# Kernel tuning notes

Hardware: AMD Instinct MI355X
Metric: run time of the kernel (lower is better)

The kernel has to match this reference:

```python
import jax, jax.numpy as jnp
import numpy as np

HEADS = 4
HEAD_DIM = 32
NEG_SLOPE = 0.2  # PyG GATConv default

N_NODES = 100000
N_EDGES = 1600000
IN_CH = 128
N_GRAPHS = 64


def setup_inputs() -> dict:
    key = jax.random.key(0)
    ks = jax.random.split(key, 6)
    x = jax.random.normal(ks[0], (N_NODES, IN_CH), dtype=jnp.float32)
    edge_index = jax.random.randint(ks[1], (2, N_EDGES), 0, N_NODES, dtype=jnp.int32)
    batch = jnp.sort(jax.random.randint(ks[2], (N_NODES,), 0, N_GRAPHS, dtype=jnp.int32))
    # glorot-style scaling
    W = jax.random.normal(ks[3], (IN_CH, HEADS * HEAD_DIM), dtype=jnp.float32) * (1.0 / np.sqrt(IN_CH))
    att_src = jax.random.normal(ks[4], (HEADS, HEAD_DIM), dtype=jnp.float32) * (1.0 / np.sqrt(HEAD_DIM))
    att_dst = jax.random.normal(ks[5], (HEADS, HEAD_DIM), dtype=jnp.float32) * (1.0 / np.sqrt(HEAD_DIM))
    bias = jnp.zeros((HEADS * HEAD_DIM,), dtype=jnp.float32)
    return {"x": x, "edge_index": edge_index, "batch": batch,
            "W": W, "att_src": att_src, "att_dst": att_dst, "bias": bias}


def reference(x, edge_index, batch, W, att_src, att_dst, bias):
    # batch is unused (collect_embeddings=False path); kept for signature fidelity
    N = x.shape[0]
    # add self-loops (PyG GATConv default add_self_loops=True)
    loop = jnp.arange(N, dtype=edge_index.dtype)
    src = jnp.concatenate([edge_index[0], loop])  # [E+N]
    dst = jnp.concatenate([edge_index[1], loop])  # [E+N]

    # linear transform, split heads: [N, H, C]
    xt = (x @ W).reshape(N, HEADS, HEAD_DIM)
    a_src = jnp.einsum('nhc,hc->nh', xt, att_src)  # [N, H]
    a_dst = jnp.einsum('nhc,hc->nh', xt, att_dst)  # [N, H]

    # edge-wise attention logits with LeakyReLU
    alpha = a_src[src] + a_dst[dst]                # [E+N, H]
    alpha = jnp.where(alpha >= 0, alpha, NEG_SLOPE * alpha)

    # segment softmax over incoming edges of each destination node
    seg_max = jax.ops.segment_max(alpha, dst, num_segments=N)   # [N, H]
    alpha = jnp.exp(alpha - seg_max[dst])
    seg_sum = jax.ops.segment_sum(alpha, dst, num_segments=N)   # [N, H]
    alpha = alpha / (seg_sum[dst] + 1e-16)

    # weighted scatter-aggregate of source features
    msg = xt[src] * alpha[:, :, None]                            # [E+N, H, C]
    out = jax.ops.segment_sum(msg, dst, num_segments=N)          # [N, H, C]
    out = out.reshape(N, HEADS * HEAD_DIM) + bias                # concat heads
    return jax.nn.relu(out)
```

## Files before the change

kernel.cpp:

```cpp
#include <hip/hip_runtime.h>
#include <hip/hip_bf16.h>

#define HEADS 4
#define CH 128
#define NTILE 9
#define NCOLS (NTILE*16)
#define WSTRIDE 136
#define CAP 64

typedef __attribute__((ext_vector_type(8))) short short8v;
typedef __attribute__((ext_vector_type(4))) float f32x4;

static __device__ __forceinline__ unsigned short f2bf(float f) {
    __hip_bfloat16 b = __float2bfloat16(f);
    return *reinterpret_cast<unsigned short*>(&b);
}
static __device__ __forceinline__ float bf2f(unsigned short u) {
    unsigned int x = ((unsigned int)u) << 16;
    return __uint_as_float(x);
}

__global__ __launch_bounds__(256) void k_prep(
    const float* __restrict__ W, const float* __restrict__ att_src,
    const float* __restrict__ att_dst, unsigned short* __restrict__ Wt)
{
    int idx = blockIdx.x * 256 + threadIdx.x;
    if (idx >= NCOLS * WSTRIDE) return;
    int c = idx / WSTRIDE;
    int k = idx % WSTRIDE;
    float v = 0.f;
    if (k < CH) {
        if (c < CH) {
            v = W[(size_t)k * CH + c];
        } else if (c < CH + 8) {
            int q = c - CH;
            const float* att = (q < 4) ? att_src : att_dst;
            int h = q & 3;
            float s = 0.f;
            #pragma unroll
            for (int t = 0; t < 32; ++t)
                s += W[(size_t)k * CH + h * 32 + t] * att[h * 32 + t];
            v = s;
        }
    }
    Wt[idx] = f2bf(v);
}

__global__ __launch_bounds__(256, 6) void k_gemm(
    const float* __restrict__ x, const unsigned short* __restrict__ Wt,
    unsigned short* __restrict__ xt, float* __restrict__ a_src, float* __restrict__ a_dst,
    int N)
{
    __shared__ unsigned short xl[64 * CH];
    char* xb = (char*)xl;
    const int tid = threadIdx.x;
    const int blk = blockIdx.x;

    {
        const float4* x4 = (const float4*)x;
        #pragma unroll
        for (int it = 0; it < 8; ++it) {
            int i   = tid + it * 256;
            int row = i >> 5, c4 = i & 31;
            int gr  = blk * 64 + row;
            float4 v = make_float4(0.f, 0.f, 0.f, 0.f);
            if (gr < N) v = x4[(size_t)gr * 32 + c4];
            ushort4 u;
            u.x = f2bf(v.x); u.y = f2bf(v.y); u.z = f2bf(v.z); u.w = f2bf(v.w);
            int byte = (row << 8) + (c4 << 3);
            byte ^= (row & 15) << 4;
            *(ushort4*)(xb + byte) = u;
        }
    }
    __syncthreads();

    const int wv = tid >> 6;
    const int l  = tid & 63;
    const int la = l & 15;
    const int lb = l >> 4;
    const int row = wv * 16 + la;

    short8v a[4];
    #pragma unroll
    for (int ks = 0; ks < 4; ++ks) {
        int byte = (row << 8) + (ks << 6) + (lb << 4);
        byte ^= la << 4;
        a[ks] = *(const short8v*)(xb + byte);
    }
    __syncthreads();

    f32x4 acc[NTILE];
    #pragma unroll
    for (int n = 0; n < NTILE; ++n) acc[n] = (f32x4){0.f, 0.f, 0.f, 0.f};

    #pragma unroll
    for (int ks = 0; ks < 4; ++ks) {
        #pragma unroll
        for (int n = 0; n < NTILE; ++n) {
            short8v bb = *(const short8v*)&Wt[(size_t)(n * 16 + la) * WSTRIDE + ks * 32 + lb * 8];
            acc[n] = __builtin_amdgcn_mfma_f32_16x16x32_bf16(a[ks], bb, acc[n], 0, 0, 0);
        }
    }

    #pragma unroll
    for (int reg = 0; reg < 4; ++reg) {
        int r = wv * 16 + lb * 4 + reg;
        int swz = (r & 15) << 4;
        #pragma unroll
        for (int n = 0; n < 8; ++n) {
            int byte = (r << 8) + ((n * 16 + la) << 1);
            *(unsigned short*)(xb + (byte ^ swz)) = f2bf(acc[n][reg]);
        }
    }
    __syncthreads();

    {
        #pragma unroll
        for (int it = 0; it < 4; ++it) {
            int j   = tid + it * 256;
            int r   = j >> 4, g = j & 15;
            int gr  = blk * 64 + r;
            if (gr < N) {
                int byte = (r << 8) + (g << 4);
                byte ^= (r & 15) << 4;
                float4 v = *(const float4*)(xb + byte);
                ((float4*)xt)[(size_t)gr * 16 + g] = v;
            }
        }
    }

    {
        int rbase = blk * 64 + wv * 16 + lb * 4;
        #pragma unroll
        for (int reg = 0; reg < 4; ++reg) {
            int gr = rbase + reg;
            if (gr < N) {
                if (la < 4)       a_src[(size_t)gr * 4 + la]       = acc[8][reg];
                else if (la < 8)  a_dst[(size_t)gr * 4 + (la - 4)] = acc[8][reg];
            }
        }
    }
}

__global__ __launch_bounds__(256) void k_scatter(
    const int* __restrict__ ei, int E, int N,
    int* __restrict__ cursor, int* __restrict__ csr)
{
    int slice = blockIdx.x & 7;
    int c     = blockIdx.x >> 3;
    int B     = gridDim.x >> 3;
    int lo = (int)((long long)N * slice / 8);
    int hi = (int)((long long)N * (slice + 1) / 8);

    for (int i = c * 256 + threadIdx.x; i < E; i += B * 256) {
        int dst = ei[E + i];
        if (dst >= lo && dst < hi) {
            int pos = atomicAdd(&cursor[dst], 1);
            if (pos < CAP) csr[((size_t)dst << 6) + pos] = ei[i];
        }
    }
}

__global__ __launch_bounds__(256) void k_gather(
    const int* __restrict__ cursor, const int* __restrict__ csr,
    const float* __restrict__ a_src, const float* __restrict__ a_dst,
    const unsigned short* __restrict__ xt, const float* __restrict__ bias,
    float* __restrict__ out, int N)
{
    int n = blockIdx.x * 4 + (threadIdx.x >> 6);
    if (n >= N) return;
    int l   = threadIdx.x & 63;
    int grp = l >> 4;
    int q   = l & 15;
    int h   = q >> 2;

    float ad = a_dst[(size_t)n * 4 + h];
    int cnt = cursor[n];
    if (cnt > CAP) cnt = CAP;
    const size_t base = (size_t)n << 6;

    float acc[8] = {0.f,0.f,0.f,0.f,0.f,0.f,0.f,0.f};
    float wsum = 0.f;
    for (int k = grp; k < cnt; k += 4) {
        int src = csr[base + k];
        float as = a_src[(size_t)src * 4 + h];
        float lg = as + ad;
        lg = (lg >= 0.f) ? lg : 0.2f * lg;
        float w = __expf(lg);
        wsum += w;
        float4 raw = ((const float4*)xt)[(size_t)src * 16 + q];
        union { float4 f; unsigned short u[8]; } uu; uu.f = raw;
        #pragma unroll
        for (int j = 0; j < 8; ++j) acc[j] += w * bf2f(uu.u[j]);
    }
    if (grp == 0) {
        float as = a_src[(size_t)n * 4 + h];
        float lg = as + ad;
        lg = (lg >= 0.f) ? lg : 0.2f * lg;
        float w = __expf(lg);
        wsum += w;
        float4 raw = ((const float4*)xt)[(size_t)n * 16 + q];
        union { float4 f; unsigned short u[8]; } uu; uu.f = raw;
        #pragma unroll
        for (int j = 0; j < 8; ++j) acc[j] += w * bf2f(uu.u[j]);
    }

    #pragma unroll
    for (int j = 0; j < 8; ++j) {
        acc[j] += __shfl_xor(acc[j], 16, 64);
        acc[j] += __shfl_xor(acc[j], 32, 64);
    }
    wsum += __shfl_xor(wsum, 16, 64);
    wsum += __shfl_xor(wsum, 32, 64);

    if (grp == 0) {
        float inv = 1.0f / wsum;
        float4 b0 = ((const float4*)bias)[q * 2];
        float4 b1 = ((const float4*)bias)[q * 2 + 1];
        float4 v0, v1;
        v0.x = fmaxf(fmaf(acc[0], inv, b0.x), 0.f);
        v0.y = fmaxf(fmaf(acc[1], inv, b0.y), 0.f);
        v0.z = fmaxf(fmaf(acc[2], inv, b0.z), 0.f);
        v0.w = fmaxf(fmaf(acc[3], inv, b0.w), 0.f);
        v1.x = fmaxf(fmaf(acc[4], inv, b1.x), 0.f);
        v1.y = fmaxf(fmaf(acc[5], inv, b1.y), 0.f);
        v1.z = fmaxf(fmaf(acc[6], inv, b1.z), 0.f);
        v1.w = fmaxf(fmaf(acc[7], inv, b1.w), 0.f);
        ((float4*)out)[(size_t)n * 32 + q * 2]     = v0;
        ((float4*)out)[(size_t)n * 32 + q * 2 + 1] = v1;
    }
}

extern "C" void kernel_launch(void* const* d_in, const int* in_sizes, int n_in,
                              void* d_out, int out_size, void* d_ws, size_t ws_size,
                              hipStream_t stream) {
    const float* x       = (const float*)d_in[0];
    const int*   ei      = (const int*)d_in[1];
    const float* W       = (const float*)d_in[3];
    const float* att_src = (const float*)d_in[4];
    const float* att_dst = (const float*)d_in[5];
    const float* bias    = (const float*)d_in[6];

    const int N = in_sizes[0] / CH;
    const int E = in_sizes[1] / 2;
    float* out = (float*)d_out;

    char* ws = (char*)d_ws;
    size_t p = 0;
    unsigned short* Wt = (unsigned short*)(ws + p); p += (size_t)NCOLS * WSTRIDE * 2;
    unsigned short* xt = (unsigned short*)(ws + p); p += (size_t)N * CH * 2;
    float* a_src  = (float*)(ws + p); p += (size_t)N * 4 * 4;
    float* a_dst  = (float*)(ws + p); p += (size_t)N * 4 * 4;
    int*   cursor = (int*)(ws + p);   p += (size_t)N * 4;
    int*   csr    = (int*)(ws + p);   p += (size_t)N * CAP * 4;

    hipMemsetAsync(cursor, 0, (size_t)N * 4, stream);

    k_prep<<<(NCOLS * WSTRIDE + 255) / 256, 256, 0, stream>>>(W, att_src, att_dst, Wt);

    k_scatter<<<2048, 256, 0, stream>>>(ei, E, N, cursor, csr);

    k_gemm<<<(N + 63) / 64, 256, 0, stream>>>(x, Wt, xt, a_src, a_dst, N);

    k_gather<<<(N + 3) / 4, 256, 0, stream>>>(cursor, csr, a_src, a_dst,
                                              xt, bias, out, N);
}
```

Before: 191.8 us.

## Fuse edge scatter into GEMM launch and batch gather edge loads by four

The CSR scatter and the bf16 GEMM now run as one launch with disjoint block ranges, so the atomic-bound scatter and the compute-bound projection can overlap on the GPU instead of running back to back. The scatter block count drops from 2048 to 1024. In the gather, each lane group reads four neighbor indices with one int4 load and issues four independent feature and logit loads before accumulating, which raises memory-level parallelism. Invalid tail slots are masked by a zero weight and read the node's own row. The fused kernel inherits the GEMM's launch bounds and shared memory, which may limit occupancy for the scatter blocks.

```diff
diff --git a/kernel.cpp b/kernel.cpp
--- a/kernel.cpp
+++ b/kernel.cpp
@@ -46,15 +46,33 @@
     Wt[idx] = f2bf(v);
 }
 
-__global__ __launch_bounds__(256, 6) void k_gemm(
+__global__ __launch_bounds__(256, 6) void k_front(
     const float* __restrict__ x, const unsigned short* __restrict__ Wt,
     unsigned short* __restrict__ xt, float* __restrict__ a_src, float* __restrict__ a_dst,
-    int N)
+    int N, const int* __restrict__ ei, int E,
+    int* __restrict__ cursor, int* __restrict__ csr, int scatB)
 {
     __shared__ unsigned short xl[64 * CH];
     char* xb = (char*)xl;
     const int tid = threadIdx.x;
-    const int blk = blockIdx.x;
+    const int b   = blockIdx.x;
+
+    if (b < scatB) {
+        int slice = b & 7;
+        int c     = b >> 3;
+        int B     = scatB >> 3;
+        int lo = (int)((long long)N * slice / 8);
+        int hi = (int)((long long)N * (slice + 1) / 8);
+        for (int i = c * 256 + tid; i < E; i += B * 256) {
+            int dst = ei[E + i];
+            if (dst >= lo && dst < hi) {
+                int pos = atomicAdd(&cursor[dst], 1);
+                if (pos < CAP) csr[((size_t)dst << 6) + pos] = ei[i];
+            }
+        }
+        return;
+    }
+    const int blk = b - scatB;
 
     {
         const float4* x4 = (const float4*)x;
@@ -138,25 +156,6 @@
                 if (la < 4)       a_src[(size_t)gr * 4 + la]       = acc[8][reg];
                 else if (la < 8)  a_dst[(size_t)gr * 4 + (la - 4)] = acc[8][reg];
             }
-        }
-    }
-}
-
-__global__ __launch_bounds__(256) void k_scatter(
-    const int* __restrict__ ei, int E, int N,
-    int* __restrict__ cursor, int* __restrict__ csr)
-{
-    int slice = blockIdx.x & 7;
-    int c     = blockIdx.x >> 3;
-    int B     = gridDim.x >> 3;
-    int lo = (int)((long long)N * slice / 8);
-    int hi = (int)((long long)N * (slice + 1) / 8);
-
-    for (int i = c * 256 + threadIdx.x; i < E; i += B * 256) {
-        int dst = ei[E + i];
-        if (dst >= lo && dst < hi) {
-            int pos = atomicAdd(&cursor[dst], 1);
-            if (pos < CAP) csr[((size_t)dst << 6) + pos] = ei[i];
         }
     }
 }
@@ -177,22 +176,42 @@
     float ad = a_dst[(size_t)n * 4 + h];
     int cnt = cursor[n];
     if (cnt > CAP) cnt = CAP;
-    const size_t base = (size_t)n << 6;
+    const int4* bucket = (const int4*)(csr + ((size_t)n << 6));
 
     float acc[8] = {0.f,0.f,0.f,0.f,0.f,0.f,0.f,0.f};
     float wsum = 0.f;
-    for (int k = grp; k < cnt; k += 4) {
-        int src = csr[base + k];
-        float as = a_src[(size_t)src * 4 + h];
-        float lg = as + ad;
-        lg = (lg >= 0.f) ? lg : 0.2f * lg;
-        float w = __expf(lg);
-        wsum += w;
-        float4 raw = ((const float4*)xt)[(size_t)src * 16 + q];
-        union { float4 f; unsigned short u[8]; } uu; uu.f = raw;
-        #pragma unroll
-        for (int j = 0; j < 8; ++j) acc[j] += w * bf2f(uu.u[j]);
-    }
+
+    for (int k0 = grp * 4; k0 < cnt; k0 += 16) {
+        int4 s4 = bucket[k0 >> 2];
+        const int* sp = (const int*)&s4;
+        int   srcs[4];
+        float ok[4];
+        #pragma unroll
+        for (int j = 0; j < 4; ++j) {
+            bool v = (k0 + j) < cnt;
+            ok[j]   = v ? 1.f : 0.f;
+            srcs[j] = v ? sp[j] : n;
+        }
+        float as[4];
+        #pragma unroll
+        for (int j = 0; j < 4; ++j)
+            as[j] = a_src[(size_t)srcs[j] * 4 + h];
+        float4 raw[4];
+        #pragma unroll
+        for (int j = 0; j < 4; ++j)
+            raw[j] = ((const float4*)xt)[(size_t)srcs[j] * 16 + q];
+        #pragma unroll
+        for (int j = 0; j < 4; ++j) {
+            float lg = as[j] + ad;
+            lg = (lg >= 0.f) ? lg : 0.2f * lg;
+            float w = __expf(lg) * ok[j];
+            wsum += w;
+            union { float4 f; unsigned short u[8]; } uu; uu.f = raw[j];
+            #pragma unroll
+            for (int jj = 0; jj < 8; ++jj) acc[jj] += w * bf2f(uu.u[jj]);
+        }
+    }
+
     if (grp == 0) {
         float as = a_src[(size_t)n * 4 + h];
         float lg = as + ad;
@@ -258,9 +277,10 @@
 
     k_prep<<<(NCOLS * WSTRIDE + 255) / 256, 256, 0, stream>>>(W, att_src, att_dst, Wt);
 
-    k_scatter<<<2048, 256, 0, stream>>>(ei, E, N, cursor, csr);
-
-    k_gemm<<<(N + 63) / 64, 256, 0, stream>>>(x, Wt, xt, a_src, a_dst, N);
+    const int scatB      = 1024;
+    const int gemmBlocks = (N + 63) / 64;
+    k_front<<<scatB + gemmBlocks, 256, 0, stream>>>(x, Wt, xt, a_src, a_dst,
+                                                    N, ei, E, cursor, csr, scatB);
 
     k_gather<<<(N + 3) / 4, 256, 0, stream>>>(cursor, csr, a_src, a_dst,
                                               xt, bias, out, N);
```

Result: faster. 172.5 us (-10.0%).
